# Optimization experiments

Measured on AMD Instinct MI355X. Metric: run time of the kernel, lower is better.

The kernel has to match this reference:

```python
import jax, jax.numpy as jnp
import numpy as np

EMBED = 256; M = 8; DV = 32; L = 4; K = 4; SCALE = 0.5
LEVELS = [(128, 128), (64, 64), (32, 32), (16, 16)]  # (H_l, W_l), static
S_TOTAL = sum(h * w for h, w in LEVELS)  # 21760


def _linear_params(key, fan_in, fan_out):
    kw, kb = jax.random.split(key)
    lim = 1.0 / np.sqrt(fan_in)
    W = jax.random.uniform(kw, (fan_in, fan_out), minval=-lim, maxval=lim, dtype=jnp.float32)
    b = jax.random.uniform(kb, (fan_out,), minval=-lim, maxval=lim, dtype=jnp.float32)
    return W, b


def setup_inputs() -> dict:
    key = jax.random.key(0)
    ks = jax.random.split(key, 8)
    N, Q = 2, 8192
    W_off, b_off = _linear_params(ks[0], EMBED, M * L * K * 2)
    W_attn, b_attn = _linear_params(ks[1], EMBED, M * L * K)
    W_val, b_val = _linear_params(ks[2], EMBED, M * DV)
    W_out, b_out = _linear_params(ks[3], M * DV, EMBED)
    queries = jax.random.normal(ks[4], (N, Q, EMBED), dtype=jnp.float32)
    query_geometry_logits = jax.random.normal(ks[5], (N, Q, 4), dtype=jnp.float32)
    value = jax.random.normal(ks[6], (N, S_TOTAL, EMBED), dtype=jnp.float32)
    value_mask = jnp.ones((N, S_TOTAL, 1), dtype=jnp.float32)
    return {"queries": queries, "query_geometry_logits": query_geometry_logits,
            "value": value, "value_mask": value_mask,
            "W_off": W_off, "b_off": b_off, "W_attn": W_attn, "b_attn": b_attn,
            "W_val": W_val, "b_val": b_val, "W_out": W_out, "b_out": b_out}


def _bilinear(img_flat, grid, H, W):
    """grid_sample(mode=bilinear, padding=zeros, align_corners=False).
    img_flat: (B, H*W, C); grid: (B, P, 2) with (x, y) in [-1, 1]."""
    x = (grid[..., 0] + 1.0) * (W * 0.5) - 0.5
    y = (grid[..., 1] + 1.0) * (H * 0.5) - 0.5
    x0f, y0f = jnp.floor(x), jnp.floor(y)
    wx, wy = x - x0f, y - y0f
    x0, y0 = x0f.astype(jnp.int32), y0f.astype(jnp.int32)

    def gather(xi, yi, w):
        valid = (xi >= 0) & (xi < W) & (yi >= 0) & (yi < H)
        idx = jnp.clip(yi, 0, H - 1) * W + jnp.clip(xi, 0, W - 1)
        v = jnp.take_along_axis(img_flat, idx[..., None], axis=1)
        return v * (w * valid)[..., None]

    return (gather(x0, y0, (1 - wx) * (1 - wy)) + gather(x0 + 1, y0, wx * (1 - wy))
            + gather(x0, y0 + 1, (1 - wx) * wy) + gather(x0 + 1, y0 + 1, wx * wy))


def _forward(queries, query_geometry_logits, value, value_mask,
             W_off, b_off, W_attn, b_attn, W_val, b_val, W_out, b_out):
    N, Q, _ = queries.shape
    # attention weights: (N, Q, M, L*K), softmax over the L*K sampling points
    attn = jax.nn.softmax((queries @ W_attn + b_attn).reshape(N, Q, M, L * K), axis=-1)
    # sampling offsets: (N, Q, M, L*K, 2)
    deltas = (queries @ W_off + b_off).reshape(N, Q, M, L * K, 2)
    # reference boxes: sigmoid -> (cx, cy, w, h) in [0, 1]
    b_q = jax.nn.sigmoid(query_geometry_logits)
    xy, wh = b_q[..., :2], b_q[..., 2:]
    scale = wh * (1.0 / K) * SCALE                       # (N, Q, 2)
    pos = xy[:, :, None, None, :] + deltas * scale[:, :, None, None, :]  # (N,Q,M,LK,2)
    # value projection + mask
    v_masked = value_mask * (value @ W_val + b_val)      # (N, S, M*DV)
    # collapse (N, M) for per-head grid sampling
    grid = jnp.clip(2.0 * pos.transpose(0, 2, 1, 3, 4).reshape(N * M, Q, L * K, 2) - 1.0, -1.0, 1.0)
    outs, start = [], 0
    for li, (H, W) in enumerate(LEVELS):
        v_l = v_masked[:, start:start + H * W, :].reshape(N, H * W, M, DV)
        v_l = v_l.transpose(0, 2, 1, 3).reshape(N * M, H * W, DV)
        g_l = grid[:, :, K * li:K * (li + 1), :].reshape(N * M, Q * K, 2)
        s_l = _bilinear(v_l, g_l, H, W)                  # (N*M, Q*K, DV)
        outs.append(s_l.reshape(N, M, Q, K, DV))
        start += H * W
    vals = jnp.concatenate(outs, axis=3)                 # (N, M, Q, L*K, DV)
    vals = vals.transpose(0, 2, 1, 3, 4)                 # (N, Q, M, L*K, DV)
    out = jnp.sum(attn[..., None] * vals, axis=3).reshape(N, Q, M * DV)
    return out @ W_out + b_out                           # (N, Q, EMBED)


def reference(queries, query_geometry_logits, value, value_mask,
              W_off, b_off, W_attn, b_attn, W_val, b_val, W_out, b_out):
    return _forward(queries, query_geometry_logits, value, value_mask,
                    W_off, b_off, W_attn, b_attn, W_val, b_val, W_out, b_out)
```

## Files before the change

kernel.cpp:

```cpp
#include <hip/hip_runtime.h>
#include <math.h>

#define EMBED   256
#define M_HEADS 8
#define DVAL    32
#define LK      16
#define S_TOTAL 21760
#define NQ      8192
#define NROWS   (2 * NQ)
#define QBS     16

typedef __attribute__((ext_vector_type(8))) short s16x8;
typedef __attribute__((ext_vector_type(4))) float f32x4;
typedef unsigned short u16;
typedef unsigned int   u32;

__device__ __forceinline__ short f2bf(float f) {
    unsigned u = __float_as_uint(f);
    u += 0x7fffu + ((u >> 16) & 1u);
    return (short)(u >> 16);
}
__device__ __forceinline__ float bf2f(short h) {
    return __uint_as_float(((unsigned)(u16)h) << 16);
}

#define V_OFF     0
#define V_FLTS    5570560
#define PA_OFF    (V_OFF + V_FLTS)
#define PA_FLTS   6291456
#define QHI_OFF   (PA_OFF + PA_FLTS)
#define QPL_FLTS  2097152
#define QLO_OFF   (QHI_OFF + QPL_FLTS)
#define MID_OFF   (QLO_OFF + QPL_FLTS)
#define MID_FLTS  2097152
#define WHI_OFF   (MID_OFF + MID_FLTS)
#define WOA_FLTS  49152
#define WLO_OFF   (WHI_OFF + WOA_FLTS)
#define WV_OFF    (WLO_OFF + WOA_FLTS)
#define WO_OFF    (WV_OFF + 32768)

__global__ __launch_bounds__(256) void prep_kernel(
    const float* __restrict__ q,     u16* __restrict__ qh, u16* __restrict__ ql,
    const float* __restrict__ W_off, const float* __restrict__ W_attn,
    u16* __restrict__ Whi,           u16* __restrict__ Wlo,
    const float* __restrict__ W_val, u16* __restrict__ Wv,
    const float* __restrict__ W_out, u16* __restrict__ Wo)
{
    const int b = blockIdx.x;
    const int t = threadIdx.x;

    if (b < 4096) {
        const int i4 = b * 256 + t;
        const float4 v = ((const float4*)q)[i4];
        short4 h, l;
        h.x = f2bf(v.x); l.x = f2bf(v.x - bf2f(h.x));
        h.y = f2bf(v.y); l.y = f2bf(v.y - bf2f(h.y));
        h.z = f2bf(v.z); l.z = f2bf(v.z - bf2f(h.z));
        h.w = f2bf(v.w); l.w = f2bf(v.w - bf2f(h.w));
        ((short4*)qh)[i4] = h;
        ((short4*)ql)[i4] = l;
    } else if (b < 4096 + 512) {
        const int flat = (b - 4096) * 256 + t;
        const int which = flat >> 16;
        const int e = flat & 65535;
        const int k = e >> 8, c = e & 255;
        const float f = which ? W_out[k * 256 + c] : W_val[k * 256 + c];
        const int kt = k >> 5, qd = (k >> 3) & 3, j = k & 7;
        const int idx = (((kt * 256 + c) << 2) + qd) * 8 + j;
        (which ? Wo : Wv)[idx] = (u16)f2bf(f);
    } else {
        const int flat = (b - 4608) * 256 + t;
        const int k = flat / 384, c = flat - k * 384;
        const float f = (c < 256) ? W_off[k * 256 + c] : W_attn[k * 128 + (c - 256)];
        const short h = f2bf(f);
        const short lo = f2bf(f - bf2f(h));
        const int kt = k >> 5, qd = (k >> 3) & 3, j = k & 7;
        const int idx = (((kt * 384 + c) << 2) + qd) * 8 + j;
        Whi[idx] = (u16)h;
        Wlo[idx] = (u16)lo;
    }
}

__global__ __launch_bounds__(256) void vproj_kernel(
    const float* __restrict__ value,
    const float* __restrict__ vmask,
    const u16* __restrict__ Wpk,
    const float* __restrict__ b_val,
    u16* __restrict__ v_out)
{
    const int t  = threadIdx.x;
    const int w  = t >> 6, l = t & 63;
    const int c  = l & 15, qd = l >> 4;
    const int r0 = blockIdx.x * 64 + w * 16;

    f32x4 acc[16] = {};

    for (int kt = 0; kt < 8; ++kt) {
        const float* ap = value + (size_t)(r0 + c) * EMBED + kt * 32 + qd * 8;
        const float4 a0 = *(const float4*)ap;
        const float4 a1 = *(const float4*)(ap + 4);
        const s16x8 a = (s16x8){ f2bf(a0.x), f2bf(a0.y), f2bf(a0.z), f2bf(a0.w),
                                 f2bf(a1.x), f2bf(a1.y), f2bf(a1.z), f2bf(a1.w) };
        s16x8 b[16];
        #pragma unroll
        for (int nt = 0; nt < 16; ++nt)
            b[nt] = *(const s16x8*)(Wpk + (((kt * 256 + nt * 16 + c) << 2) + qd) * 8);
        #pragma unroll
        for (int nt = 0; nt < 16; ++nt)
            acc[nt] = __builtin_amdgcn_mfma_f32_16x16x32_bf16(a, b[nt], acc[nt], 0, 0, 0);
    }

    #pragma unroll
    for (int r = 0; r < 4; ++r) {
        const int grow = r0 + qd * 4 + r;
        const int n = (grow >= S_TOTAL) ? 1 : 0;
        const int s = grow - n * S_TOTAL;
        const float mk = vmask[grow];
        #pragma unroll
        for (int nt = 0; nt < 16; ++nt) {
            const int col = nt * 16 + c;
            const int hm = col >> 5, d = col & 31;
            v_out[((size_t)(n * M_HEADS + hm) * S_TOTAL + s) * DVAL + d] =
                (u16)f2bf((acc[nt][r] + b_val[col]) * mk);
        }
    }
}

__global__ __launch_bounds__(256) void qproj_kernel(
    const u16* __restrict__ q_hi, const u16* __restrict__ q_lo,
    const float* __restrict__ qgl,
    const u16* __restrict__ Whi, const u16* __restrict__ Wlo,
    const float* __restrict__ b_off, const float* __restrict__ b_attn,
    float* __restrict__ pa)
{
    __shared__ float s_off[32][260];
    __shared__ float s_attn[32][132];
    __shared__ float s_geom[32][4];

    const int t  = threadIdx.x;
    const int w  = t >> 6, l = t & 63;
    const int c  = l & 15, qd = l >> 4;
    const int row0 = blockIdx.x * 32;
    const int c0 = w * 96;

    if (t < 32) {
        const float* g = &qgl[(size_t)(row0 + t) * 4];
        s_geom[t][0] = 1.f / (1.f + __expf(-g[0]));
        s_geom[t][1] = 1.f / (1.f + __expf(-g[1]));
        s_geom[t][2] = (1.f / (1.f + __expf(-g[2]))) * 0.125f;
        s_geom[t][3] = (1.f / (1.f + __expf(-g[3]))) * 0.125f;
    }

    f32x4 acc[2][6] = {};

    for (int kt = 0; kt < 8; ++kt) {
        s16x8 ah[2], al[2], bh[6], bl[6];
        #pragma unroll
        for (int mt = 0; mt < 2; ++mt) {
            const size_t ao = (size_t)(row0 + mt * 16 + c) * EMBED + kt * 32 + qd * 8;
            ah[mt] = *(const s16x8*)(q_hi + ao);
            al[mt] = *(const s16x8*)(q_lo + ao);
        }
        #pragma unroll
        for (int nt = 0; nt < 6; ++nt) {
            const int idx = (((kt * 384 + c0 + nt * 16 + c) << 2) + qd) * 8;
            bh[nt] = *(const s16x8*)(Whi + idx);
            bl[nt] = *(const s16x8*)(Wlo + idx);
        }
        #pragma unroll
        for (int mt = 0; mt < 2; ++mt)
            #pragma unroll
            for (int nt = 0; nt < 6; ++nt) {
                acc[mt][nt] = __builtin_amdgcn_mfma_f32_16x16x32_bf16(ah[mt], bh[nt], acc[mt][nt], 0, 0, 0);
                acc[mt][nt] = __builtin_amdgcn_mfma_f32_16x16x32_bf16(ah[mt], bl[nt], acc[mt][nt], 0, 0, 0);
                acc[mt][nt] = __builtin_amdgcn_mfma_f32_16x16x32_bf16(al[mt], bh[nt], acc[mt][nt], 0, 0, 0);
            }
    }

    #pragma unroll
    for (int mt = 0; mt < 2; ++mt)
        #pragma unroll
        for (int nt = 0; nt < 6; ++nt) {
            const int col = c0 + nt * 16 + c;
            #pragma unroll
            for (int r = 0; r < 4; ++r) {
                const int row = mt * 16 + qd * 4 + r;
                if (col < 256) s_off[row][col] = acc[mt][nt][r] + b_off[col];
                else           s_attn[row][col - 256] = acc[mt][nt][r] + b_attn[col - 256];
            }
        }
    __syncthreads();

    {
        const int qi = t >> 3, hm = t & 7;
        float* a = &s_attn[qi][hm * LK];
        float mx = a[0];
        #pragma unroll
        for (int i = 1; i < LK; ++i) mx = fmaxf(mx, a[i]);
        float s = 0.f;
        #pragma unroll
        for (int i = 0; i < LK; ++i) { const float e = __expf(a[i] - mx); a[i] = e; s += e; }
        const float inv = 1.f / s;
        #pragma unroll
        for (int i = 0; i < LK; ++i) a[i] *= inv;
    }
    __syncthreads();

    for (int p = t; p < 32 * 128; p += 256) {
        const int qi = p >> 7;
        const int pt = p & 127;
        const int lvl = (pt & 15) >> 2;
        const float Wl = (float)(128 >> lvl);
        const float px = fmaf(s_off[qi][2 * pt + 0], s_geom[qi][2], s_geom[qi][0]);
        const float py = fmaf(s_off[qi][2 * pt + 1], s_geom[qi][3], s_geom[qi][1]);
        const float gx = fminf(fmaxf(2.f * px - 1.f, -1.f), 1.f);
        const float gy = fminf(fmaxf(2.f * py - 1.f, -1.f), 1.f);
        const float x = (gx + 1.f) * (Wl * 0.5f) - 0.5f;
        const float y = (gy + 1.f) * (Wl * 0.5f) - 0.5f;
        const size_t idx = ((size_t)(row0 + qi) * 128 + pt) * 3;
        pa[idx + 0] = x;
        pa[idx + 1] = y;
        pa[idx + 2] = s_attn[qi][pt];
    }
}

__global__ __launch_bounds__(256) void sample_kernel(
    const float* __restrict__ pa,
    const u16* __restrict__ v_tab,
    u16* __restrict__ mid)
{
    __shared__ int4   s_idx[QBS * 17];
    __shared__ float4 s_w[QBS * 17];

    const int t    = threadIdx.x;
    const int m    = blockIdx.x & 7;
    const int rest = blockIdx.x >> 3;
    const int qc   = rest & 511;
    const int n    = rest >> 9;
    const int q0   = qc * QBS;

    {
        const int qi = t >> 4, lk = t & 15;
        const int lvl   = lk >> 2;
        const int Wl    = 128 >> lvl;
        const int start = (lvl == 0) ? 0 : (lvl == 1) ? 16384 : (lvl == 2) ? 20480 : 21504;

        const size_t prow = ((size_t)(n * NQ + q0 + qi)) * 128 + m * 16 + lk;
        const float x  = pa[prow * 3 + 0];
        const float y  = pa[prow * 3 + 1];
        const float aw = pa[prow * 3 + 2];

        const float x0f = floorf(x), y0f = floorf(y);
        const int   x0 = (int)x0f, y0 = (int)y0f;
        const float wx = x - x0f, wy = y - y0f;

        const float vx0 = (x0 >= 0) ? 1.f : 0.f;
        const float vx1 = (x0 + 1 <= Wl - 1) ? 1.f : 0.f;
        const float vy0 = (y0 >= 0) ? 1.f : 0.f;
        const float vy1 = (y0 + 1 <= Wl - 1) ? 1.f : 0.f;

        const int xc0 = max(x0, 0);
        const int xc1 = min(x0 + 1, Wl - 1);
        const int yc0 = max(y0, 0);
        const int yc1 = min(y0 + 1, Wl - 1);

        const int e = qi * 17 + lk;
        s_idx[e] = make_int4((start + yc0 * Wl + xc0) * DVAL,
                             (start + yc0 * Wl + xc1) * DVAL,
                             (start + yc1 * Wl + xc0) * DVAL,
                             (start + yc1 * Wl + xc1) * DVAL);
        s_w[e] = make_float4(aw * (1.f - wx) * (1.f - wy) * vx0 * vy0,
                             aw * wx * (1.f - wy) * vx1 * vy0,
                             aw * (1.f - wx) * wy * vx0 * vy1,
                             aw * wx * wy * vx1 * vy1);
    }
    __syncthreads();

    const int g = t >> 4, dp = t & 15;
    const u16* __restrict__ vbp =
        v_tab + (size_t)(n * M_HEADS + m) * S_TOTAL * DVAL + 2 * dp;

    float acc0 = 0.f, acc1 = 0.f;
    #pragma unroll
    for (int lk = 0; lk < LK; ++lk) {
        const int4   id = s_idx[g * 17 + lk];
        const float4 w  = s_w[g * 17 + lk];
        const u32 u0 = *(const u32*)(vbp + id.x);
        const u32 u1 = *(const u32*)(vbp + id.y);
        const u32 u2 = *(const u32*)(vbp + id.z);
        const u32 u3 = *(const u32*)(vbp + id.w);
        acc0 = fmaf(w.x, __uint_as_float(u0 << 16), acc0);
        acc1 = fmaf(w.x, __uint_as_float(u0 & 0xffff0000u), acc1);
        acc0 = fmaf(w.y, __uint_as_float(u1 << 16), acc0);
        acc1 = fmaf(w.y, __uint_as_float(u1 & 0xffff0000u), acc1);
        acc0 = fmaf(w.z, __uint_as_float(u2 << 16), acc0);
        acc1 = fmaf(w.z, __uint_as_float(u2 & 0xffff0000u), acc1);
        acc0 = fmaf(w.w, __uint_as_float(u3 << 16), acc0);
        acc1 = fmaf(w.w, __uint_as_float(u3 & 0xffff0000u), acc1);
    }

    const u32 packed = ((u32)(u16)f2bf(acc1) << 16) | (u32)(u16)f2bf(acc0);
    *(u32*)(mid + ((size_t)(n * NQ + q0 + g)) * EMBED + m * DVAL + 2 * dp) = packed;
}

__global__ __launch_bounds__(256) void out_kernel(
    const u16* __restrict__ mid,
    const u16* __restrict__ Wpk,
    const float* __restrict__ b_out,
    float* __restrict__ out)
{
    const int t  = threadIdx.x;
    const int w  = t >> 6, l = t & 63;
    const int c  = l & 15, qd = l >> 4;
    const int r0 = blockIdx.y * 128 + w * 32;
    const int c0 = blockIdx.x * 64;

    f32x4 acc[2][4] = {};

    for (int kt = 0; kt < 8; ++kt) {
        s16x8 a[2], b[4];
        #pragma unroll
        for (int mt = 0; mt < 2; ++mt)
            a[mt] = *(const s16x8*)(mid + (size_t)(r0 + mt * 16 + c) * EMBED + kt * 32 + qd * 8);
        #pragma unroll
        for (int nt = 0; nt < 4; ++nt)
            b[nt] = *(const s16x8*)(Wpk + (((kt * 256 + c0 + nt * 16 + c) << 2) + qd) * 8);
        #pragma unroll
        for (int mt = 0; mt < 2; ++mt)
            #pragma unroll
            for (int nt = 0; nt < 4; ++nt)
                acc[mt][nt] = __builtin_amdgcn_mfma_f32_16x16x32_bf16(a[mt], b[nt], acc[mt][nt], 0, 0, 0);
    }

    #pragma unroll
    for (int mt = 0; mt < 2; ++mt)
        #pragma unroll
        for (int r = 0; r < 4; ++r) {
            const int row = r0 + mt * 16 + qd * 4 + r;
            #pragma unroll
            for (int nt = 0; nt < 4; ++nt) {
                const int col = c0 + nt * 16 + c;
                out[(size_t)row * EMBED + col] = acc[mt][nt][r] + b_out[col];
            }
        }
}

extern "C" void kernel_launch(void* const* d_in, const int* in_sizes, int n_in,
                              void* d_out, int out_size, void* d_ws, size_t ws_size,
                              hipStream_t stream) {
    (void)in_sizes; (void)n_in; (void)out_size; (void)ws_size;

    const float* queries = (const float*)d_in[0];
    const float* qgl     = (const float*)d_in[1];
    const float* value   = (const float*)d_in[2];
    const float* vmask   = (const float*)d_in[3];
    const float* W_off   = (const float*)d_in[4];
    const float* b_off   = (const float*)d_in[5];
    const float* W_attn  = (const float*)d_in[6];
    const float* b_attn  = (const float*)d_in[7];
    const float* W_val   = (const float*)d_in[8];
    const float* b_val   = (const float*)d_in[9];
    const float* W_out   = (const float*)d_in[10];
    const float* b_out   = (const float*)d_in[11];

    float* ws   = (float*)d_ws;
    u16*  v_ws  = (u16*)(ws + V_OFF);
    float* pa   = ws + PA_OFF;
    u16*  q_hi  = (u16*)(ws + QHI_OFF);
    u16*  q_lo  = (u16*)(ws + QLO_OFF);
    u16*  mid   = (u16*)(ws + MID_OFF);
    u16*  whi   = (u16*)(ws + WHI_OFF);
    u16*  wlo   = (u16*)(ws + WLO_OFF);
    u16*  wvpk  = (u16*)(ws + WV_OFF);
    u16*  wopk  = (u16*)(ws + WO_OFF);
    float* outp = (float*)d_out;

    prep_kernel<<<4992, 256, 0, stream>>>(queries, q_hi, q_lo,
                                          W_off, W_attn, whi, wlo,
                                          W_val, wvpk, W_out, wopk);

    vproj_kernel<<<680, 256, 0, stream>>>(value, vmask, wvpk, b_val, v_ws);
    qproj_kernel<<<NROWS / 32, 256, 0, stream>>>(q_hi, q_lo, qgl, whi, wlo,
                                                 b_off, b_attn, pa);
    sample_kernel<<<2 * (NQ / QBS) * M_HEADS, 256, 0, stream>>>(pa, v_ws, mid);
    out_kernel<<<dim3(4, 128), 256, 0, stream>>>(mid, wopk, b_out, outp);
}
```

Before: 223.2 us.

## Fuse query bf16 hi/lo split into qproj and double-buffer vproj loads

Removes the query hi/lo bf16 split pass from the prep kernel and does the split inside qproj while loading fp32 queries directly, so the q_hi/q_lo workspace buffers are never written and read back. The vproj kernel gains register double-buffering: the A and B fragments for the next k-tile are loaded before the MFMAs on the current one run, with a launch_bounds occupancy hint. The trade is more conversion ALU work per qproj block and higher register pressure in vproj.

```diff
diff --git a/kernel.cpp b/kernel.cpp
--- a/kernel.cpp
+++ b/kernel.cpp
@@ -28,10 +28,7 @@
 #define V_FLTS    5570560
 #define PA_OFF    (V_OFF + V_FLTS)
 #define PA_FLTS   6291456
-#define QHI_OFF   (PA_OFF + PA_FLTS)
-#define QPL_FLTS  2097152
-#define QLO_OFF   (QHI_OFF + QPL_FLTS)
-#define MID_OFF   (QLO_OFF + QPL_FLTS)
+#define MID_OFF   (PA_OFF + PA_FLTS)
 #define MID_FLTS  2097152
 #define WHI_OFF   (MID_OFF + MID_FLTS)
 #define WOA_FLTS  49152
@@ -40,7 +37,6 @@
 #define WO_OFF    (WV_OFF + 32768)
 
 __global__ __launch_bounds__(256) void prep_kernel(
-    const float* __restrict__ q,     u16* __restrict__ qh, u16* __restrict__ ql,
     const float* __restrict__ W_off, const float* __restrict__ W_attn,
     u16* __restrict__ Whi,           u16* __restrict__ Wlo,
     const float* __restrict__ W_val, u16* __restrict__ Wv,
@@ -49,18 +45,8 @@
     const int b = blockIdx.x;
     const int t = threadIdx.x;
 
-    if (b < 4096) {
-        const int i4 = b * 256 + t;
-        const float4 v = ((const float4*)q)[i4];
-        short4 h, l;
-        h.x = f2bf(v.x); l.x = f2bf(v.x - bf2f(h.x));
-        h.y = f2bf(v.y); l.y = f2bf(v.y - bf2f(h.y));
-        h.z = f2bf(v.z); l.z = f2bf(v.z - bf2f(h.z));
-        h.w = f2bf(v.w); l.w = f2bf(v.w - bf2f(h.w));
-        ((short4*)qh)[i4] = h;
-        ((short4*)ql)[i4] = l;
-    } else if (b < 4096 + 512) {
-        const int flat = (b - 4096) * 256 + t;
+    if (b < 512) {
+        const int flat = b * 256 + t;
         const int which = flat >> 16;
         const int e = flat & 65535;
         const int k = e >> 8, c = e & 255;
@@ -69,7 +55,7 @@
         const int idx = (((kt * 256 + c) << 2) + qd) * 8 + j;
         (which ? Wo : Wv)[idx] = (u16)f2bf(f);
     } else {
-        const int flat = (b - 4608) * 256 + t;
+        const int flat = (b - 512) * 256 + t;
         const int k = flat / 384, c = flat - k * 384;
         const float f = (c < 256) ? W_off[k * 256 + c] : W_attn[k * 128 + (c - 256)];
         const short h = f2bf(f);
@@ -81,7 +67,7 @@
     }
 }
 
-__global__ __launch_bounds__(256) void vproj_kernel(
+__global__ __launch_bounds__(256, 2) void vproj_kernel(
     const float* __restrict__ value,
     const float* __restrict__ vmask,
     const u16* __restrict__ Wpk,
@@ -93,21 +79,38 @@
     const int c  = l & 15, qd = l >> 4;
     const int r0 = blockIdx.x * 64 + w * 16;
 
+    const float* __restrict__ aptr = value + (size_t)(r0 + c) * EMBED + qd * 8;
+
     f32x4 acc[16] = {};
 
+    s16x8 bcur[16], bnxt[16];
+    float4 a0c, a1c, a0n, a1n;
+
+    a0c = *(const float4*)(aptr);
+    a1c = *(const float4*)(aptr + 4);
+    #pragma unroll
+    for (int nt = 0; nt < 16; ++nt)
+        bcur[nt] = *(const s16x8*)(Wpk + (((nt * 16 + c) << 2) + qd) * 8);
+
+    #pragma unroll
     for (int kt = 0; kt < 8; ++kt) {
-        const float* ap = value + (size_t)(r0 + c) * EMBED + kt * 32 + qd * 8;
-        const float4 a0 = *(const float4*)ap;
-        const float4 a1 = *(const float4*)(ap + 4);
-        const s16x8 a = (s16x8){ f2bf(a0.x), f2bf(a0.y), f2bf(a0.z), f2bf(a0.w),
-                                 f2bf(a1.x), f2bf(a1.y), f2bf(a1.z), f2bf(a1.w) };
-        s16x8 b[16];
+        if (kt < 7) {
+            a0n = *(const float4*)(aptr + (kt + 1) * 32);
+            a1n = *(const float4*)(aptr + (kt + 1) * 32 + 4);
+            #pragma unroll
+            for (int nt = 0; nt < 16; ++nt)
+                bnxt[nt] = *(const s16x8*)(Wpk + ((((kt + 1) * 256 + nt * 16 + c) << 2) + qd) * 8);
+        }
+        const s16x8 a = (s16x8){ f2bf(a0c.x), f2bf(a0c.y), f2bf(a0c.z), f2bf(a0c.w),
+                                 f2bf(a1c.x), f2bf(a1c.y), f2bf(a1c.z), f2bf(a1c.w) };
         #pragma unroll
         for (int nt = 0; nt < 16; ++nt)
-            b[nt] = *(const s16x8*)(Wpk + (((kt * 256 + nt * 16 + c) << 2) + qd) * 8);
-        #pragma unroll
-        for (int nt = 0; nt < 16; ++nt)
-            acc[nt] = __builtin_amdgcn_mfma_f32_16x16x32_bf16(a, b[nt], acc[nt], 0, 0, 0);
+            acc[nt] = __builtin_amdgcn_mfma_f32_16x16x32_bf16(a, bcur[nt], acc[nt], 0, 0, 0);
+        if (kt < 7) {
+            a0c = a0n; a1c = a1n;
+            #pragma unroll
+            for (int nt = 0; nt < 16; ++nt) bcur[nt] = bnxt[nt];
+        }
     }
 
     #pragma unroll
@@ -127,7 +130,7 @@
 }
 
 __global__ __launch_bounds__(256) void qproj_kernel(
-    const u16* __restrict__ q_hi, const u16* __restrict__ q_lo,
+    const float* __restrict__ queries,
     const float* __restrict__ qgl,
     const u16* __restrict__ Whi, const u16* __restrict__ Wlo,
     const float* __restrict__ b_off, const float* __restrict__ b_attn,
@@ -157,9 +160,16 @@
         s16x8 ah[2], al[2], bh[6], bl[6];
         #pragma unroll
         for (int mt = 0; mt < 2; ++mt) {
-            const size_t ao = (size_t)(row0 + mt * 16 + c) * EMBED + kt * 32 + qd * 8;
-            ah[mt] = *(const s16x8*)(q_hi + ao);
-            al[mt] = *(const s16x8*)(q_lo + ao);
+            const float* qp = queries + (size_t)(row0 + mt * 16 + c) * EMBED + kt * 32 + qd * 8;
+            const float4 v0 = *(const float4*)qp;
+            const float4 v1 = *(const float4*)(qp + 4);
+            const short h0 = f2bf(v0.x), h1 = f2bf(v0.y), h2 = f2bf(v0.z), h3 = f2bf(v0.w);
+            const short h4 = f2bf(v1.x), h5 = f2bf(v1.y), h6 = f2bf(v1.z), h7 = f2bf(v1.w);
+            ah[mt] = (s16x8){ h0, h1, h2, h3, h4, h5, h6, h7 };
+            al[mt] = (s16x8){ f2bf(v0.x - bf2f(h0)), f2bf(v0.y - bf2f(h1)),
+                              f2bf(v0.z - bf2f(h2)), f2bf(v0.w - bf2f(h3)),
+                              f2bf(v1.x - bf2f(h4)), f2bf(v1.y - bf2f(h5)),
+                              f2bf(v1.z - bf2f(h6)), f2bf(v1.w - bf2f(h7)) };
         }
         #pragma unroll
         for (int nt = 0; nt < 6; ++nt) {
@@ -366,8 +376,6 @@
     float* ws   = (float*)d_ws;
     u16*  v_ws  = (u16*)(ws + V_OFF);
     float* pa   = ws + PA_OFF;
-    u16*  q_hi  = (u16*)(ws + QHI_OFF);
-    u16*  q_lo  = (u16*)(ws + QLO_OFF);
     u16*  mid   = (u16*)(ws + MID_OFF);
     u16*  whi   = (u16*)(ws + WHI_OFF);
     u16*  wlo   = (u16*)(ws + WLO_OFF);
@@ -375,12 +383,11 @@
     u16*  wopk  = (u16*)(ws + WO_OFF);
     float* outp = (float*)d_out;
 
-    prep_kernel<<<4992, 256, 0, stream>>>(queries, q_hi, q_lo,
-                                          W_off, W_attn, whi, wlo,
-                                          W_val, wvpk, W_out, wopk);
+    prep_kernel<<<896, 256, 0, stream>>>(W_off, W_attn, whi, wlo,
+                                         W_val, wvpk, W_out, wopk);
 
     vproj_kernel<<<680, 256, 0, stream>>>(value, vmask, wvpk, b_val, v_ws);
-    qproj_kernel<<<NROWS / 32, 256, 0, stream>>>(q_hi, q_lo, qgl, whi, wlo,
+    qproj_kernel<<<NROWS / 32, 256, 0, stream>>>(queries, qgl, whi, wlo,
                                                  b_off, b_attn, pa);
     sample_kernel<<<2 * (NQ / QBS) * M_HEADS, 256, 0, stream>>>(pa, v_ws, mid);
     out_kernel<<<dim3(4, 128), 256, 0, stream>>>(mid, wopk, b_out, outp);
```

Measured after the change: 213.7 us. 1.04x faster.
